# Performance work log

Hardware: AMD Instinct MI355X
Metric: run time of the kernel (lower is better)

The kernel has to match this reference:

```python
import jax, jax.numpy as jnp
import numpy as np

N, C, T, V, K = 64, 64, 300, 25, 3
EPS = 1e-5


def setup_inputs() -> dict:
    key = jax.random.key(0)
    ks = jax.random.split(key, 4)
    x = jax.random.normal(ks[0], (N, C, T, V), dtype=jnp.float32)
    A = jax.random.uniform(ks[1], (K, V, V), dtype=jnp.float32)
    # per-subset 1x1 conv weights: W[k] maps C_in -> C_out, plus bias b[k]
    W = jax.random.normal(ks[2], (K, C, C), dtype=jnp.float32) * (1.0 / np.sqrt(C))
    b = jax.random.normal(ks[3], (K, C), dtype=jnp.float32) * 0.01
    gamma = jnp.ones((C,), dtype=jnp.float32)
    beta = jnp.zeros((C,), dtype=jnp.float32)
    return {"x": x, "A": A, "W": W, "b": b, "gamma": gamma, "beta": beta}


def reference(x, A, W, b, gamma, beta):
    # y = sum_k conv1x1_k( einsum('nctv,vw->nctw', x, A[k]) )
    # conv1x1 over (C,T,V) with kernel 1 == channel matmul; fuse subsets via one einsum.
    y = jnp.einsum('nctv,kvw,koc->notw', x, A, W)
    y = y + jnp.sum(b, axis=0)[None, :, None, None]
    # BatchNorm2d in training mode: batch statistics over (N, T, V) per channel
    mean = jnp.mean(y, axis=(0, 2, 3), keepdims=True)
    var = jnp.mean(jnp.square(y - mean), axis=(0, 2, 3), keepdims=True)
    y = gamma[None, :, None, None] * (y - mean) * jax.lax.rsqrt(var + EPS) + beta[None, :, None, None]
    # residual (in_channels == out_channels -> identity) + relu
    return jax.nn.relu(y + x)
```

## Files before the change

### kernel.cpp

```cpp
#include <hip/hip_runtime.h>
#include <hip/hip_bf16.h>

#define N_ 64
#define C_ 64
#define T_ 300
#define V_ 25
#define K_ 3
#define TT 12
#define NTILE 25
#define NBLK 1600
#define XROW 384
#define WP 72
#define ATP 40
#define EPS_ 1e-5f

typedef __bf16 bf16_t;
typedef __bf16 bf16x4 __attribute__((ext_vector_type(4)));
typedef __bf16 bf16x8 __attribute__((ext_vector_type(8)));
typedef float f32x4 __attribute__((ext_vector_type(4)));
typedef float f32x4u __attribute__((ext_vector_type(4), aligned(4)));

static __device__ __forceinline__ bf16_t tobf(float f) { return (bf16_t)f; }
static __device__ __forceinline__ int emask(int c) { return ((c & 3) << 3) | ((c & 8) << 2); }

union SmemU {
  struct { bf16_t W[3 * 64 * WP]; bf16_t At[3 * 32 * ATP]; } wa;
  bf16_t xs[64 * XROW];
};

struct Frags {
  bf16x8 wfrag[6];
  bf16x8 afrag[3][2];
  int fK[4], fS5[4];
  float bs[4];
  int obase;
};

static __device__ __forceinline__ void stage_wa(
    const float* __restrict__ A, const float* __restrict__ W, SmemU& sm, int tid) {
  for (int m = tid; m < 3072; m += 256) {
    f32x4 v4 = *(reinterpret_cast<const f32x4*>(W) + m);
    int f = m << 2;
    int k = f >> 12, o = (f >> 6) & 63, c = f & 63;
    bf16x4 h;
    h[0] = tobf(v4[0]); h[1] = tobf(v4[1]); h[2] = tobf(v4[2]); h[3] = tobf(v4[3]);
    *reinterpret_cast<bf16x4*>(&sm.wa.W[(k * 64 + o) * WP + c]) = h;
  }
  for (int i = tid; i < 3072; i += 256) {
    int k = i >> 10, r = i & 1023, w = r >> 5, v = r & 31;
    float val = (v < V_ && w < V_) ? A[k * 625 + v * 25 + w] : 0.f;
    sm.wa.At[(k * 32 + w) * ATP + v] = tobf(val);
  }
}

static __device__ __forceinline__ void read_frags(
    const SmemU& sm, const float* __restrict__ b, int wv, int l15, int lg, Frags& F) {
  const int o = wv * 16 + l15;
  #pragma unroll
  for (int k = 0; k < 3; ++k)
    #pragma unroll
    for (int ch = 0; ch < 2; ++ch)
      F.wfrag[k * 2 + ch] =
          *reinterpret_cast<const bf16x8*>(&sm.wa.W[(k * 64 + o) * WP + ch * 32 + lg * 8]);
  #pragma unroll
  for (int k = 0; k < 3; ++k)
    #pragma unroll
    for (int wh = 0; wh < 2; ++wh)
      F.afrag[k][wh] =
          *reinterpret_cast<const bf16x8*>(&sm.wa.At[(k * 32 + wh * 16 + l15) * ATP + lg * 8]);
  const int crow = 8 * (l15 >> 2) + (l15 & 3);
  #pragma unroll
  for (int q = 0; q < 4; ++q) {
    int c = ((q >> 1) * 32) + ((q & 1) * 4) + crow;
    int em = emask(c);
    F.fK[q] = c * XROW + ((lg * 8) ^ (em & 24));
    F.fS5[q] = em & 32;
  }
  F.obase = wv * 16 + lg * 4;
  #pragma unroll
  for (int r = 0; r < 4; ++r)
    F.bs[r] = b[F.obase + r] + b[64 + F.obase + r] + b[128 + F.obase + r];
}

static __device__ __forceinline__ void stage_x(
    const float* __restrict__ x, SmemU& sm, int n, int t0, int tid) {
  const float* xb = x + (size_t)n * 480000 + (size_t)t0 * 25;
  for (int i = tid; i < 64 * TT * 8; i += 256) {
    int c = i / (TT * 8), r = i - c * (TT * 8);
    int t = r >> 3, vb = r & 7;
    bf16x4 h;
    if (vb < 6) {
      f32x4u v4 = *reinterpret_cast<const f32x4u*>(xb + (size_t)c * 7500 + t * 25 + vb * 4);
      h[0] = tobf(v4[0]); h[1] = tobf(v4[1]); h[2] = tobf(v4[2]); h[3] = tobf(v4[3]);
    } else if (vb == 6) {
      float s = xb[(size_t)c * 7500 + t * 25 + 24];
      h[0] = tobf(s); h[1] = tobf(0.f); h[2] = tobf(0.f); h[3] = tobf(0.f);
    } else {
      h[0] = tobf(0.f); h[1] = tobf(0.f); h[2] = tobf(0.f); h[3] = tobf(0.f);
    }
    *reinterpret_cast<bf16x4*>(&sm.xs[c * XROW + (((t << 5) + vb * 4) ^ emask(c))]) = h;
  }
}

static __device__ __forceinline__ void compute_t(
    const bf16_t* xs, const Frags& F, int t, int wh, f32x4& acc0, f32x4& acc1) {
  bf16x8 xf[4];
  #pragma unroll
  for (int q = 0; q < 4; ++q)
    xf[q] = *reinterpret_cast<const bf16x8*>(xs + F.fK[q] + ((t << 5) ^ F.fS5[q]));
  acc0 = f32x4{0.f, 0.f, 0.f, 0.f};
  acc1 = f32x4{0.f, 0.f, 0.f, 0.f};
  #pragma unroll
  for (int k = 0; k < 3; ++k) {
    #pragma unroll
    for (int ch = 0; ch < 2; ++ch) {
      f32x4 zero = {0.f, 0.f, 0.f, 0.f};
      f32x4 dP = __builtin_amdgcn_mfma_f32_16x16x32_bf16(xf[ch * 2 + 0], F.afrag[k][wh], zero, 0, 0, 0);
      f32x4 dQ = __builtin_amdgcn_mfma_f32_16x16x32_bf16(xf[ch * 2 + 1], F.afrag[k][wh], zero, 0, 0, 0);
      bf16x8 zf;
      zf[0] = tobf(dP[0]); zf[1] = tobf(dP[1]); zf[2] = tobf(dP[2]); zf[3] = tobf(dP[3]);
      zf[4] = tobf(dQ[0]); zf[5] = tobf(dQ[1]); zf[6] = tobf(dQ[2]); zf[7] = tobf(dQ[3]);
      if (ch == 0)
        acc0 = __builtin_amdgcn_mfma_f32_16x16x32_bf16(F.wfrag[k * 2 + ch], zf, acc0, 0, 0, 0);
      else
        acc1 = __builtin_amdgcn_mfma_f32_16x16x32_bf16(F.wfrag[k * 2 + ch], zf, acc1, 0, 0, 0);
    }
  }
}

__global__ __launch_bounds__(256, 3) void k1_compute(
    const float* __restrict__ x, const float* __restrict__ A,
    const float* __restrict__ W, const float* __restrict__ b,
    float* __restrict__ y, float* __restrict__ part) {
  __shared__ __align__(16) SmemU sm;
  __shared__ float stats[2][64];

  const int bid = (blockIdx.x & 7) * (NBLK / 8) + (blockIdx.x >> 3);
  const int n = bid / NTILE;
  const int t0 = (bid - n * NTILE) * TT;
  const int tid = threadIdx.x;
  const int lane = tid & 63;
  const int wv = tid >> 6;
  const int l15 = lane & 15;
  const int lg = lane >> 4;

  stage_wa(A, W, sm, tid);
  __syncthreads();
  Frags F;
  read_frags(sm, b, wv, l15, lg, F);
  __syncthreads();
  stage_x(x, sm, n, t0, tid);
  __syncthreads();

  float lsum[4] = {0.f, 0.f, 0.f, 0.f}, lsq[4] = {0.f, 0.f, 0.f, 0.f};
  const int w_lo = l15, w_hi = 16 + l15;
  float* yb = y + (size_t)n * 480000 + (size_t)t0 * 25;

  #pragma unroll 2
  for (int t = 0; t < TT; ++t) {
    #pragma unroll
    for (int wh = 0; wh < 2; ++wh) {
      f32x4 acc0, acc1;
      compute_t(sm.xs, F, t, wh, acc0, acc1);
      const int w = wh ? w_hi : w_lo;
      if (w < V_) {
        #pragma unroll
        for (int r = 0; r < 4; ++r) {
          float val = acc0[r] + acc1[r] + F.bs[r];
          lsum[r] += val;
          lsq[r] += val * val;
          yb[(size_t)(F.obase + r) * 7500 + t * 25 + w] = val;
        }
      }
    }
  }

  #pragma unroll
  for (int d = 1; d < 16; d <<= 1) {
    #pragma unroll
    for (int r = 0; r < 4; ++r) {
      lsum[r] += __shfl_xor(lsum[r], d);
      lsq[r]  += __shfl_xor(lsq[r], d);
    }
  }
  if (l15 == 0) {
    #pragma unroll
    for (int r = 0; r < 4; ++r) {
      stats[0][F.obase + r] = lsum[r];
      stats[1][F.obase + r] = lsq[r];
    }
  }
  __syncthreads();
  if (tid < 128) part[(size_t)bid * 128 + tid] = stats[tid >> 6][tid & 63];
}

__global__ __launch_bounds__(256) void k2_stats(
    const float* __restrict__ part,
    const float* __restrict__ gamma, const float* __restrict__ beta,
    float* __restrict__ ss) {
  const int o = blockIdx.x;
  const int tid = threadIdx.x;
  double s = 0.0, q = 0.0;
  for (int i = tid; i < NBLK; i += 256) {
    s += (double)part[(size_t)i * 128 + o];
    q += (double)part[(size_t)i * 128 + 64 + o];
  }
  __shared__ double sd[256], qd[256];
  sd[tid] = s; qd[tid] = q;
  __syncthreads();
  for (int step = 128; step > 0; step >>= 1) {
    if (tid < step) { sd[tid] += sd[tid + step]; qd[tid] += qd[tid + step]; }
    __syncthreads();
  }
  if (tid == 0) {
    const double cnt = 480000.0;
    double mean = sd[0] / cnt;
    double var = qd[0] / cnt - mean * mean;
    float inv = rsqrtf((float)var + EPS_);
    float sc = gamma[o] * inv;
    float sh = beta[o] - (float)mean * sc;
    ss[2 * o] = sc;
    ss[2 * o + 1] = sh;
  }
}

__global__ __launch_bounds__(256) void k3_finish(
    const float* __restrict__ x, const float* __restrict__ ss,
    float* __restrict__ y) {
  const int p = blockIdx.x;
  const int c = p & 63;
  const float sc = ss[2 * c];
  const float sh = ss[2 * c + 1];
  const float4* xv = reinterpret_cast<const float4*>(x + (size_t)p * 7500);
  float4* yv = reinterpret_cast<float4*>(y + (size_t)p * 7500);
  for (int i = threadIdx.x; i < 1875; i += 256) {
    float4 a = yv[i];
    float4 b4 = xv[i];
    float4 o;
    o.x = fmaxf(sc * a.x + sh + b4.x, 0.f);
    o.y = fmaxf(sc * a.y + sh + b4.y, 0.f);
    o.z = fmaxf(sc * a.z + sh + b4.z, 0.f);
    o.w = fmaxf(sc * a.w + sh + b4.w, 0.f);
    yv[i] = o;
  }
}

extern "C" void kernel_launch(void* const* d_in, const int* in_sizes, int n_in,
                              void* d_out, int out_size, void* d_ws, size_t ws_size,
                              hipStream_t stream) {
  const float* x     = (const float*)d_in[0];
  const float* A     = (const float*)d_in[1];
  const float* W     = (const float*)d_in[2];
  const float* b     = (const float*)d_in[3];
  const float* gamma = (const float*)d_in[4];
  const float* beta  = (const float*)d_in[5];
  float* y = (float*)d_out;

  float* part = (float*)d_ws;
  float* ss   = part + (size_t)NBLK * 128;

  k1_compute<<<NBLK, 256, 0, stream>>>(x, A, W, b, y, part);
  k2_stats<<<64, 256, 0, stream>>>(part, gamma, beta, ss);
  k3_finish<<<4096, 256, 0, stream>>>(x, ss, y);
}
```

Before: 157.7 us.

## Double k1 block size, splitting time steps across two wave groups

The compute kernel now launches 512 threads per block. Waves 0-3 and waves 4-7 each handle the same output-channel slices for half of the 12 time steps. Per-block statistics are reduced across the two halves in shared memory. Staging loops use the larger stride, and the x fragment load is hoisted out of the wh loop. The aim is more waves per CU, to hide the latency of staging and the dependent MFMA chain, at the cost of higher register and occupancy pressure from the 6-block launch bound.

After: 395.7 us. 2.51x slower.

```diff
diff --git a/kernel.cpp b/kernel.cpp
--- a/kernel.cpp
+++ b/kernel.cpp
@@ -12,6 +12,7 @@
 #define XROW 384
 #define WP 72
 #define ATP 40
+#define NTHR 512
 #define EPS_ 1e-5f
 
 typedef __bf16 bf16_t;
@@ -38,7 +39,7 @@
 
 static __device__ __forceinline__ void stage_wa(
     const float* __restrict__ A, const float* __restrict__ W, SmemU& sm, int tid) {
-  for (int m = tid; m < 3072; m += 256) {
+  for (int m = tid; m < 3072; m += NTHR) {
     f32x4 v4 = *(reinterpret_cast<const f32x4*>(W) + m);
     int f = m << 2;
     int k = f >> 12, o = (f >> 6) & 63, c = f & 63;
@@ -46,7 +47,7 @@
     h[0] = tobf(v4[0]); h[1] = tobf(v4[1]); h[2] = tobf(v4[2]); h[3] = tobf(v4[3]);
     *reinterpret_cast<bf16x4*>(&sm.wa.W[(k * 64 + o) * WP + c]) = h;
   }
-  for (int i = tid; i < 3072; i += 256) {
+  for (int i = tid; i < 3072; i += NTHR) {
     int k = i >> 10, r = i & 1023, w = r >> 5, v = r & 31;
     float val = (v < V_ && w < V_) ? A[k * 625 + v * 25 + w] : 0.f;
     sm.wa.At[(k * 32 + w) * ATP + v] = tobf(val);
@@ -54,8 +55,8 @@
 }
 
 static __device__ __forceinline__ void read_frags(
-    const SmemU& sm, const float* __restrict__ b, int wv, int l15, int lg, Frags& F) {
-  const int o = wv * 16 + l15;
+    const SmemU& sm, const float* __restrict__ b, int ob, int l15, int lg, Frags& F) {
+  const int o = ob * 16 + l15;
   #pragma unroll
   for (int k = 0; k < 3; ++k)
     #pragma unroll
@@ -76,7 +77,7 @@
     F.fK[q] = c * XROW + ((lg * 8) ^ (em & 24));
     F.fS5[q] = em & 32;
   }
-  F.obase = wv * 16 + lg * 4;
+  F.obase = ob * 16 + lg * 4;
   #pragma unroll
   for (int r = 0; r < 4; ++r)
     F.bs[r] = b[F.obase + r] + b[64 + F.obase + r] + b[128 + F.obase + r];
@@ -85,7 +86,7 @@
 static __device__ __forceinline__ void stage_x(
     const float* __restrict__ x, SmemU& sm, int n, int t0, int tid) {
   const float* xb = x + (size_t)n * 480000 + (size_t)t0 * 25;
-  for (int i = tid; i < 64 * TT * 8; i += 256) {
+  for (int i = tid; i < 64 * TT * 8; i += NTHR) {
     int c = i / (TT * 8), r = i - c * (TT * 8);
     int t = r >> 3, vb = r & 7;
     bf16x4 h;
@@ -102,12 +103,8 @@
   }
 }
 
-static __device__ __forceinline__ void compute_t(
-    const bf16_t* xs, const Frags& F, int t, int wh, f32x4& acc0, f32x4& acc1) {
-  bf16x8 xf[4];
-  #pragma unroll
-  for (int q = 0; q < 4; ++q)
-    xf[q] = *reinterpret_cast<const bf16x8*>(xs + F.fK[q] + ((t << 5) ^ F.fS5[q]));
+static __device__ __forceinline__ void compute_wh(
+    const bf16x8* xf, const Frags& F, int wh, f32x4& acc0, f32x4& acc1) {
   acc0 = f32x4{0.f, 0.f, 0.f, 0.f};
   acc1 = f32x4{0.f, 0.f, 0.f, 0.f};
   #pragma unroll
@@ -128,12 +125,12 @@
   }
 }
 
-__global__ __launch_bounds__(256, 3) void k1_compute(
+__global__ __launch_bounds__(NTHR, 6) void k1_compute(
     const float* __restrict__ x, const float* __restrict__ A,
     const float* __restrict__ W, const float* __restrict__ b,
     float* __restrict__ y, float* __restrict__ part) {
   __shared__ __align__(16) SmemU sm;
-  __shared__ float stats[2][64];
+  __shared__ float stats2[2][2][64];
 
   const int bid = (blockIdx.x & 7) * (NBLK / 8) + (blockIdx.x >> 3);
   const int n = bid / NTILE;
@@ -141,13 +138,15 @@
   const int tid = threadIdx.x;
   const int lane = tid & 63;
   const int wv = tid >> 6;
+  const int ob = wv & 3;
+  const int th = wv >> 2;
   const int l15 = lane & 15;
   const int lg = lane >> 4;
 
   stage_wa(A, W, sm, tid);
   __syncthreads();
   Frags F;
-  read_frags(sm, b, wv, l15, lg, F);
+  read_frags(sm, b, ob, l15, lg, F);
   __syncthreads();
   stage_x(x, sm, n, t0, tid);
   __syncthreads();
@@ -157,11 +156,16 @@
   float* yb = y + (size_t)n * 480000 + (size_t)t0 * 25;
 
   #pragma unroll 2
-  for (int t = 0; t < TT; ++t) {
+  for (int tl = 0; tl < 6; ++tl) {
+    const int t = th * 6 + tl;
+    bf16x8 xf[4];
+    #pragma unroll
+    for (int q = 0; q < 4; ++q)
+      xf[q] = *reinterpret_cast<const bf16x8*>(sm.xs + F.fK[q] + ((t << 5) ^ F.fS5[q]));
     #pragma unroll
     for (int wh = 0; wh < 2; ++wh) {
       f32x4 acc0, acc1;
-      compute_t(sm.xs, F, t, wh, acc0, acc1);
+      compute_wh(xf, F, wh, acc0, acc1);
       const int w = wh ? w_hi : w_lo;
       if (w < V_) {
         #pragma unroll
@@ -186,12 +190,14 @@
   if (l15 == 0) {
     #pragma unroll
     for (int r = 0; r < 4; ++r) {
-      stats[0][F.obase + r] = lsum[r];
-      stats[1][F.obase + r] = lsq[r];
-    }
-  }
-  __syncthreads();
-  if (tid < 128) part[(size_t)bid * 128 + tid] = stats[tid >> 6][tid & 63];
+      stats2[0][th][F.obase + r] = lsum[r];
+      stats2[1][th][F.obase + r] = lsq[r];
+    }
+  }
+  __syncthreads();
+  if (tid < 128)
+    part[(size_t)bid * 128 + tid] =
+        stats2[tid >> 6][0][tid & 63] + stats2[tid >> 6][1][tid & 63];
 }
 
 __global__ __launch_bounds__(256) void k2_stats(
@@ -259,7 +265,7 @@
   float* part = (float*)d_ws;
   float* ss   = part + (size_t)NBLK * 128;
 
-  k1_compute<<<NBLK, 256, 0, stream>>>(x, A, W, b, y, part);
+  k1_compute<<<NBLK, NTHR, 0, stream>>>(x, A, W, b, y, part);
   k2_stats<<<64, 256, 0, stream>>>(part, gamma, beta, ss);
   k3_finish<<<4096, 256, 0, stream>>>(x, ss, y);
 }
```
